# Kernel optimization log

Measured on AMD Instinct MI355X. Metric: run time of the kernel, lower is better.

## Reference

```python
import jax, jax.numpy as jnp
import numpy as np

B, L, DM, DS, DC, E = 2, 1024, 1024, 16, 4, 2
DI = E * DM          # d_inner = 2048
DR = DM // 16        # dt_rank = 64
EPS = 1e-5


def setup_inputs() -> dict:
    key = jax.random.key(0)
    ks = jax.random.split(key, 8)
    s = lambda k, shp, sc: jax.random.normal(k, shp, jnp.float32) * sc
    return {
        "x": s(ks[0], (B, L, DM), 1.0),
        "norm_w": jnp.ones((DM,), jnp.float32),
        "in_proj_w": s(ks[1], (2 * DI, DM), 0.02),
        "conv_w": s(ks[2], (DI, 1, DC), 0.1),        # depthwise kernel [O=DI, I=1, W=DC]
        "conv_b": s(ks[3], (DI,), 0.02),
        "x_proj_w": s(ks[4], (DR + 2 * DS, DI), 0.02),
        "dt_proj_w": s(ks[5], (DI, DR), 0.02),
        "dt_proj_b": s(ks[6], (DI,), 0.02),
        "A_log": jnp.log(jnp.broadcast_to(jnp.arange(1, DS + 1, dtype=jnp.float32), (DI, DS))),
        "D": jnp.ones((DI,), jnp.float32),
        "out_proj_w": s(ks[7], (DM, DI), 0.02),
    }


def reference(x, norm_w, in_proj_w, conv_w, conv_b, x_proj_w,
              dt_proj_w, dt_proj_b, A_log, D, out_proj_w):
    # RMSNorm
    u = x * jax.lax.rsqrt(jnp.mean(x * x, axis=-1, keepdims=True) + EPS) * norm_w

    # in_proj -> [B, L, 2*DI], split into ssm branch and gate
    xz = jnp.einsum('bld,ed->ble', u, in_proj_w)
    xin, z = jnp.split(xz, 2, axis=-1)

    # causal depthwise conv along L + SiLU
    xc = jnp.transpose(xin, (0, 2, 1))                      # [B, DI, L]
    xc = jnp.pad(xc, ((0, 0), (0, 0), (DC - 1, 0)))
    xc = jax.lax.conv_general_dilated(xc, conv_w, (1,), 'VALID',
                                      feature_group_count=DI)  # [B, DI, L]
    xc = jax.nn.silu(xc + conv_b[None, :, None])
    xc = jnp.transpose(xc, (0, 2, 1))                       # [B, L, DI]

    # input-dependent dt, B, C
    dbl = jnp.einsum('bld,ed->ble', xc, x_proj_w)           # [B, L, DR+2*DS]
    dt, Bm, Cm = jnp.split(dbl, [DR, DR + DS], axis=-1)
    delta = jax.nn.softplus(jnp.einsum('blr,dr->bld', dt, dt_proj_w) + dt_proj_b)  # [B,L,DI]

    A = -jnp.exp(A_log)                                     # [DI, DS]
    dA = jnp.exp(delta[..., None] * A)                      # [B, L, DI, DS]
    dBu = delta[..., None] * Bm[:, :, None, :] * xc[..., None]  # [B, L, DI, DS]

    # selective scan: h_t = dA_t * h_{t-1} + dBu_t ; y_t = <h_t, C_t>
    def step(h, inp):
        da, dbu, c = inp
        h = da * h + dbu                                    # [B, DI, DS]
        return h, jnp.einsum('bdn,bn->bd', h, c)

    h0 = jnp.zeros((B, DI, DS), x.dtype)
    _, ys = jax.lax.scan(step, h0,
                         (jnp.swapaxes(dA, 0, 1),
                          jnp.swapaxes(dBu, 0, 1),
                          jnp.swapaxes(Cm, 0, 1)))
    y = jnp.swapaxes(ys, 0, 1) + xc * D                     # [B, L, DI]

    out = jnp.einsum('bld,ed->ble', y * jax.nn.silu(z), out_proj_w)
    return out + x  # residual
```

## Files before the change

kernel.cpp:

```cpp
#include <hip/hip_runtime.h>
#include <math.h>

#define B_   2
#define L_   1024
#define DM   1024
#define DS   16
#define DC   4
#define DI   2048
#define DR   64
#define NTOK (B_*L_)
#define EPSF 1e-5f
#define NC   16
#define CL   (L_/NC)
#define SPLITS 8

typedef __bf16 bf16_t;
typedef bf16_t bf16x4 __attribute__((ext_vector_type(4)));
typedef bf16_t bf16x8 __attribute__((ext_vector_type(8)));
typedef float  f32x4  __attribute__((ext_vector_type(4)));

__device__ __forceinline__ float siluf(float x){ return x / (1.f + __expf(-x)); }
__device__ __forceinline__ float softplusf(float x){ return (x > 20.f) ? x : log1pf(__expf(x)); }

__device__ __forceinline__ void gload_lds16(const void* g, void* l) {
    __builtin_amdgcn_global_load_lds(
        (const __attribute__((address_space(1))) void*)g,
        (__attribute__((address_space(3))) void*)l, 16, 0, 0);
}

__global__ __launch_bounds__(256) void rmsnorm_k(const float* __restrict__ x,
                                                 const float* __restrict__ w,
                                                 bf16_t* __restrict__ uh,
                                                 bf16_t* __restrict__ ul)
{
    int row = blockIdx.x;
    int t = threadIdx.x;
    float4 v = ((const float4*)(x + (size_t)row*DM))[t];
    float ss = v.x*v.x + v.y*v.y + v.z*v.z + v.w*v.w;
    #pragma unroll
    for (int off = 32; off > 0; off >>= 1) ss += __shfl_xor(ss, off, 64);
    __shared__ float sred[4];
    if ((t & 63) == 0) sred[t >> 6] = ss;
    __syncthreads();
    ss = sred[0] + sred[1] + sred[2] + sred[3];
    float rs = rsqrtf(ss * (1.f/(float)DM) + EPSF);
    float4 wv = ((const float4*)w)[t];
    float o[4];
    o[0] = v.x*rs*wv.x; o[1] = v.y*rs*wv.y; o[2] = v.z*rs*wv.z; o[3] = v.w*rs*wv.w;
    bf16x4 hv, lv;
    #pragma unroll
    for (int j = 0; j < 4; ++j) {
        bf16_t h = (bf16_t)o[j];
        hv[j] = h;
        lv[j] = (bf16_t)(o[j] - (float)h);
    }
    *(bf16x4*)(uh + (size_t)row*DM + t*4) = hv;
    *(bf16x4*)(ul + (size_t)row*DM + t*4) = lv;
}

__global__ __launch_bounds__(256) void split_k(const float* __restrict__ s,
                                               bf16_t* __restrict__ h,
                                               bf16_t* __restrict__ l, int n4)
{
    int i = blockIdx.x * 256 + threadIdx.x;
    if (i >= n4) return;
    float4 v = ((const float4*)s)[i];
    float o[4] = {v.x, v.y, v.z, v.w};
    bf16x4 hv, lv;
    #pragma unroll
    for (int j = 0; j < 4; ++j) {
        bf16_t hh = (bf16_t)o[j];
        hv[j] = hh;
        lv[j] = (bf16_t)(o[j] - (float)hh);
    }
    ((bf16x4*)h)[i] = hv;
    ((bf16x4*)l)[i] = lv;
}

__global__ __launch_bounds__(256) void splitx_k(const float* __restrict__ s,
                                                bf16_t* __restrict__ h,
                                                bf16_t* __restrict__ l)
{
    int i = blockIdx.x * 256 + threadIdx.x;
    int row = i >> 9;
    bf16x4 hv, lv;
    if (row < 96) {
        float4 v = ((const float4*)s)[i];
        float o[4] = {v.x, v.y, v.z, v.w};
        #pragma unroll
        for (int j = 0; j < 4; ++j) {
            bf16_t hh = (bf16_t)o[j];
            hv[j] = hh;
            lv[j] = (bf16_t)(o[j] - (float)hh);
        }
    } else {
        #pragma unroll
        for (int j = 0; j < 4; ++j) { hv[j] = (bf16_t)0.f; lv[j] = (bf16_t)0.f; }
    }
    ((bf16x4*)h)[i] = hv;
    ((bf16x4*)l)[i] = lv;
}

template<int BN, int EPI, bool SK>
__global__ __launch_bounds__(256) void gemm_mfma(
    const bf16_t* __restrict__ Ah, const bf16_t* __restrict__ Al,
    const bf16_t* __restrict__ Bh, const bf16_t* __restrict__ Bl,
    float* __restrict__ C, int ldc,
    const float* __restrict__ res, const float* __restrict__ bias,
    int M, int N, int K, int kspl)
{
    constexpr int NJ   = BN / 32;
    constexpr int WN   = BN / 2;
    constexpr int ACH  = 8;
    constexpr int BCH  = BN / 16;
    constexpr int NCH  = 2*ACH + 2*BCH;
    constexpr int PERW = NCH / 4;
    constexpr int AOFF_L = 128*32;
    constexpr int BOFF_H = 2*128*32;
    constexpr int BOFF_L = 2*128*32 + BN*32;
    constexpr int BUFSZ  = 2*128*32 + 2*BN*32;

    __shared__ bf16_t lds[2*BUFSZ];

    int t = threadIdx.x;
    int w = t >> 6, lane = t & 63;
    int wr = w >> 1, wc = w & 1;
    int m0 = blockIdx.y * 128;
    int n0 = SK ? 0 : blockIdx.x * BN;
    int k0beg = SK ? blockIdx.x * kspl : 0;
    int nst = (SK ? kspl : K) >> 5;
    float* Cp = C;
    if (SK) Cp += (size_t)blockIdx.x * M * BN;

    f32x4 acc[4][NJ];
    #pragma unroll
    for (int i = 0; i < 4; ++i)
        #pragma unroll
        for (int j = 0; j < NJ; ++j)
            acc[i][j] = (f32x4){0.f, 0.f, 0.f, 0.f};

    int lrow = lane >> 2;
    int lcol = (lane & 3) * 8;
    int ar   = wr*64 + (lane & 15);
    int br   = wc*WN + (lane & 15);
    int koff = (lane >> 4) * 8;

    auto STAGE = [&](int buf, int k0) {
        int base = buf ? BUFSZ : 0;
        #pragma unroll
        for (int q = 0; q < PERW; ++q) {
            int ch = w * PERW + q;
            const bf16_t* g; int le;
            if (ch < ACH) {
                int cc = ch;
                g  = Ah + (size_t)(m0 + cc*16 + lrow)*K + k0 + lcol;
                le = cc*512 + lane*8;
            } else if (ch < 2*ACH) {
                int cc = ch - ACH;
                g  = Al + (size_t)(m0 + cc*16 + lrow)*K + k0 + lcol;
                le = AOFF_L + cc*512 + lane*8;
            } else if (ch < 2*ACH + BCH) {
                int cc = ch - 2*ACH;
                g  = Bh + (size_t)(n0 + cc*16 + lrow)*K + k0 + lcol;
                le = BOFF_H + cc*512 + lane*8;
            } else {
                int cc = ch - 2*ACH - BCH;
                g  = Bl + (size_t)(n0 + cc*16 + lrow)*K + k0 + lcol;
                le = BOFF_L + cc*512 + lane*8;
            }
            gload_lds16(g, &lds[base + le]);
        }
    };

    STAGE(0, k0beg);
    __syncthreads();
    int cur = 0;
    for (int s = 0; s < nst; ++s) {
        int k0 = k0beg + (s << 5);
        if (s + 1 < nst) STAGE(cur ^ 1, k0 + 32);
        int base = cur ? BUFSZ : 0;

        bf16x8 ah[4], al4[4], bh[NJ], bl4[NJ];
        #pragma unroll
        for (int i = 0; i < 4; ++i) {
            ah[i]  = *(const bf16x8*)&lds[base + (ar + i*16)*32 + koff];
            al4[i] = *(const bf16x8*)&lds[base + AOFF_L + (ar + i*16)*32 + koff];
        }
        #pragma unroll
        for (int j = 0; j < NJ; ++j) {
            bh[j]  = *(const bf16x8*)&lds[base + BOFF_H + (br + j*16)*32 + koff];
            bl4[j] = *(const bf16x8*)&lds[base + BOFF_L + (br + j*16)*32 + koff];
        }
        #pragma unroll
        for (int i = 0; i < 4; ++i)
            #pragma unroll
            for (int j = 0; j < NJ; ++j) {
                acc[i][j] = __builtin_amdgcn_mfma_f32_16x16x32_bf16(ah[i],  bh[j],  acc[i][j], 0, 0, 0);
                acc[i][j] = __builtin_amdgcn_mfma_f32_16x16x32_bf16(al4[i], bh[j],  acc[i][j], 0, 0, 0);
                acc[i][j] = __builtin_amdgcn_mfma_f32_16x16x32_bf16(ah[i],  bl4[j], acc[i][j], 0, 0, 0);
            }
        __syncthreads();
        cur ^= 1;
    }

    int rb = m0 + wr*64 + (lane >> 4)*4;
    int cb = n0 + wc*WN + (lane & 15);
    #pragma unroll
    for (int i = 0; i < 4; ++i)
        #pragma unroll
        for (int j = 0; j < NJ; ++j) {
            int col = cb + j*16;
            float bcol = (EPI == 1) ? bias[col] : 0.f;
            #pragma unroll
            for (int r = 0; r < 4; ++r) {
                int row = rb + i*16 + r;
                float v = acc[i][j][r];
                if (EPI == 1) v = softplusf(v + bcol);
                if (EPI == 2) v += res[(size_t)row*ldc + col];
                Cp[(size_t)row*ldc + col] = v;
            }
        }
}

__global__ __launch_bounds__(256) void xproj_reduce(const float* __restrict__ parts,
                                                    bf16_t* __restrict__ dth,
                                                    bf16_t* __restrict__ dtl,
                                                    float* __restrict__ bc)
{
    int idx = blockIdx.x * 256 + threadIdx.x;
    int m  = idx >> 5;
    int c  = (idx & 31) * 4;
    float4 s = {0.f, 0.f, 0.f, 0.f};
    #pragma unroll
    for (int sp = 0; sp < SPLITS; ++sp) {
        float4 v = *(const float4*)(parts + ((size_t)sp*NTOK + m)*128 + c);
        s.x += v.x; s.y += v.y; s.z += v.z; s.w += v.w;
    }
    if (c < 64) {
        float o[4] = {s.x, s.y, s.z, s.w};
        bf16x4 hv, lv;
        #pragma unroll
        for (int j = 0; j < 4; ++j) {
            bf16_t hh = (bf16_t)o[j];
            hv[j] = hh;
            lv[j] = (bf16_t)(o[j] - (float)hh);
        }
        *(bf16x4*)(dth + (size_t)m*DR + c) = hv;
        *(bf16x4*)(dtl + (size_t)m*DR + c) = lv;
    } else if (c < 96) {
        *(float4*)(bc + (size_t)m*32 + (c - 64)) = s;
    }
}

__global__ __launch_bounds__(256) void conv_silu_k(const float* __restrict__ xz,
                                                   const float* __restrict__ cw,
                                                   const float* __restrict__ cb,
                                                   bf16_t* __restrict__ xch,
                                                   bf16_t* __restrict__ xcl)
{
    int idx = blockIdx.x * 256 + threadIdx.x;
    int d4 = idx & (DI/4 - 1);
    int m  = idx >> 9;
    int l  = m & (L_ - 1);
    int d  = d4 * 4;

    float4 w0 = *(const float4*)(cw + (size_t)(d+0)*DC);
    float4 w1 = *(const float4*)(cw + (size_t)(d+1)*DC);
    float4 w2 = *(const float4*)(cw + (size_t)(d+2)*DC);
    float4 w3 = *(const float4*)(cw + (size_t)(d+3)*DC);
    float wr0[4] = {w0.x,w0.y,w0.z,w0.w};
    float wr1[4] = {w1.x,w1.y,w1.z,w1.w};
    float wr2[4] = {w2.x,w2.y,w2.z,w2.w};
    float wr3[4] = {w3.x,w3.y,w3.z,w3.w};
    float4 bias = *(const float4*)(cb + d);
    float a0 = bias.x, a1 = bias.y, a2 = bias.z, a3 = bias.w;

    #pragma unroll
    for (int j = 0; j < DC; ++j) {
        int tt = l - (DC-1) + j;
        if (tt < 0) continue;
        float4 xv = *(const float4*)(xz + (size_t)(m - l + tt)*(2*DI) + d);
        a0 = fmaf(wr0[j], xv.x, a0);
        a1 = fmaf(wr1[j], xv.y, a1);
        a2 = fmaf(wr2[j], xv.z, a2);
        a3 = fmaf(wr3[j], xv.w, a3);
    }
    float o[4] = { siluf(a0), siluf(a1), siluf(a2), siluf(a3) };
    bf16x4 hv, lv;
    #pragma unroll
    for (int j = 0; j < 4; ++j) {
        bf16_t hh = (bf16_t)o[j];
        hv[j] = hh;
        lv[j] = (bf16_t)(o[j] - (float)hh);
    }
    *(bf16x4*)(xch + (size_t)m*DI + d) = hv;
    *(bf16x4*)(xcl + (size_t)m*DI + d) = lv;
}

__global__ __launch_bounds__(256) void scan_p1(const float* __restrict__ delta,
                                               const bf16_t* __restrict__ xch,
                                               const bf16_t* __restrict__ xcl,
                                               const float* __restrict__ bc,
                                               const float* __restrict__ A_log,
                                               float* __restrict__ Pbuf,
                                               float* __restrict__ Hbuf)
{
    __shared__ float Bsh[CL][16];
    int t = threadIdx.x;
    int blk = blockIdx.x;
    int d = (blk & 7) * 256 + t;
    int c = (blk >> 3) & (NC - 1);
    int b = blk >> 7;
    int m0 = b * L_ + c * CL;

    for (int i = t; i < CL*16; i += 256)
        Bsh[i >> 4][i & 15] = bc[(size_t)(m0 + (i >> 4))*32 + (i & 15)];
    __syncthreads();

    float A[16], h[16];
    #pragma unroll
    for (int j = 0; j < 4; ++j) {
        float4 al = *(const float4*)(A_log + (size_t)d*DS + j*4);
        A[j*4+0] = -__expf(al.x); A[j*4+1] = -__expf(al.y);
        A[j*4+2] = -__expf(al.z); A[j*4+3] = -__expf(al.w);
    }
    #pragma unroll
    for (int n = 0; n < 16; ++n) h[n] = 0.f;
    float S = 0.f;

    #pragma unroll 4
    for (int tt = 0; tt < CL; ++tt) {
        int m = m0 + tt;
        float dv = delta[(size_t)m*DI + d];
        float xv = (float)xch[(size_t)m*DI + d] + (float)xcl[(size_t)m*DI + d];
        float dx = dv * xv;
        S += dv;
        #pragma unroll
        for (int n = 0; n < 16; ++n) {
            float dA = __expf(dv * A[n]);
            h[n] = fmaf(dA, h[n], Bsh[tt][n] * dx);
        }
    }

    size_t o = ((size_t)((b*NC + c)*DI) + d) * DS;
    #pragma unroll
    for (int j = 0; j < 4; ++j) {
        float4 pv, hv;
        pv.x = __expf(A[j*4+0]*S); pv.y = __expf(A[j*4+1]*S);
        pv.z = __expf(A[j*4+2]*S); pv.w = __expf(A[j*4+3]*S);
        hv.x = h[j*4+0]; hv.y = h[j*4+1]; hv.z = h[j*4+2]; hv.w = h[j*4+3];
        *(float4*)(Pbuf + o + j*4) = pv;
        *(float4*)(Hbuf + o + j*4) = hv;
    }
}

__global__ __launch_bounds__(256) void scan_p2(float* Pbuf, const float* __restrict__ Hbuf)
{
    int idx = blockIdx.x * 256 + threadIdx.x;
    int n = idx & 15;
    int d = (idx >> 4) & (DI - 1);
    int b = idx >> 15;
    float h = 0.f;
    #pragma unroll
    for (int c = 0; c < NC; ++c) {
        size_t o = ((size_t)((b*NC + c)*DI) + d) * DS + n;
        float p  = Pbuf[o];
        float hh = Hbuf[o];
        Pbuf[o] = h;
        h = fmaf(p, h, hh);
    }
}

__global__ __launch_bounds__(256) void scan_p3(const float* __restrict__ delta,
                                               const float* __restrict__ xz,
                                               const bf16_t* __restrict__ xch,
                                               const bf16_t* __restrict__ xcl,
                                               const float* __restrict__ bc,
                                               const float* __restrict__ A_log,
                                               const float* __restrict__ Dp,
                                               const float* __restrict__ h0buf,
                                               bf16_t* __restrict__ gh,
                                               bf16_t* __restrict__ gl)
{
    __shared__ float Bsh[CL][16];
    __shared__ float Csh[CL][16];
    int t = threadIdx.x;
    int blk = blockIdx.x;
    int d = (blk & 7) * 256 + t;
    int c = (blk >> 3) & (NC - 1);
    int b = blk >> 7;
    int m0 = b * L_ + c * CL;

    for (int i = t; i < CL*16; i += 256) {
        int tt = i >> 4, n = i & 15;
        size_t ro = (size_t)(m0 + tt)*32;
        Bsh[tt][n] = bc[ro + n];
        Csh[tt][n] = bc[ro + 16 + n];
    }
    __syncthreads();

    float A[16], h[16];
    #pragma unroll
    for (int j = 0; j < 4; ++j) {
        float4 al = *(const float4*)(A_log + (size_t)d*DS + j*4);
        A[j*4+0] = -__expf(al.x); A[j*4+1] = -__expf(al.y);
        A[j*4+2] = -__expf(al.z); A[j*4+3] = -__expf(al.w);
    }
    size_t o = ((size_t)((b*NC + c)*DI) + d) * DS;
    #pragma unroll
    for (int j = 0; j < 4; ++j) {
        float4 hv = *(const float4*)(h0buf + o + j*4);
        h[j*4+0] = hv.x; h[j*4+1] = hv.y; h[j*4+2] = hv.z; h[j*4+3] = hv.w;
    }
    float Dreg = Dp[d];

    for (int t0 = 0; t0 < CL; t0 += 4) {
        float dv[4], xv[4], zv[4];
        #pragma unroll
        for (int q = 0; q < 4; ++q) {
            int m = m0 + t0 + q;
            dv[q] = delta[(size_t)m*DI + d];
            xv[q] = (float)xch[(size_t)m*DI + d] + (float)xcl[(size_t)m*DI + d];
            zv[q] = xz[(size_t)m*(2*DI) + DI + d];
        }
        #pragma unroll
        for (int q = 0; q < 4; ++q) {
            int tt = t0 + q, m = m0 + tt;
            float dx = dv[q] * xv[q];
            float y = 0.f;
            #pragma unroll
            for (int n = 0; n < 16; ++n) {
                float dA = __expf(dv[q] * A[n]);
                h[n] = fmaf(dA, h[n], Bsh[tt][n] * dx);
                y = fmaf(h[n], Csh[tt][n], y);
            }
            float gv = (y + xv[q]*Dreg) * siluf(zv[q]);
            bf16_t hh = (bf16_t)gv;
            gh[(size_t)m*DI + d] = hh;
            gl[(size_t)m*DI + d] = (bf16_t)(gv - (float)hh);
        }
    }
}

extern "C" void kernel_launch(void* const* d_in, const int* in_sizes, int n_in,
                              void* d_out, int out_size, void* d_ws, size_t ws_size,
                              hipStream_t stream)
{
    const float* x         = (const float*)d_in[0];
    const float* norm_w    = (const float*)d_in[1];
    const float* in_proj_w = (const float*)d_in[2];
    const float* conv_w    = (const float*)d_in[3];
    const float* conv_b    = (const float*)d_in[4];
    const float* x_proj_w  = (const float*)d_in[5];
    const float* dt_proj_w = (const float*)d_in[6];
    const float* dt_proj_b = (const float*)d_in[7];
    const float* A_log     = (const float*)d_in[8];
    const float* Dp        = (const float*)d_in[9];
    const float* out_proj_w= (const float*)d_in[10];
    float* out = (float*)d_out;

    char* p = (char*)d_ws;
    float*  xz    = (float*)p;  p += (size_t)NTOK*2*DI*4;
    bf16_t* xch   = (bf16_t*)p; p += (size_t)NTOK*DI*2;
    bf16_t* xcl   = (bf16_t*)p; p += (size_t)NTOK*DI*2;
    float*  delta = (float*)p;  p += (size_t)NTOK*DI*4;
    float*  bc    = (float*)p;  p += (size_t)NTOK*32*4;
    bf16_t* dth   = (bf16_t*)p; p += (size_t)NTOK*DR*2;
    bf16_t* dtl   = (bf16_t*)p; p += (size_t)NTOK*DR*2;
    float*  Hbuf  = (float*)p;  p += (size_t)B_*NC*DI*DS*4;
    float*  Pbuf  = (float*)p;  p += (size_t)B_*NC*DI*DS*4;
    char*   Wreg  = p;          p += (size_t)2*DI*DM*2*2;
    bf16_t* wxh   = (bf16_t*)p; p += (size_t)128*DI*2;
    bf16_t* wxl   = (bf16_t*)p; p += (size_t)128*DI*2;
    bf16_t* wdth  = (bf16_t*)p; p += (size_t)DI*DR*2;
    bf16_t* wdtl  = (bf16_t*)p; p += (size_t)DI*DR*2;

    bf16_t* uh  = (bf16_t*)Pbuf;
    bf16_t* ul  = uh + (size_t)NTOK*DM;
    bf16_t* wih = (bf16_t*)Wreg;
    bf16_t* wil = wih + (size_t)2*DI*DM;
    bf16_t* gh  = (bf16_t*)Wreg;
    bf16_t* gl  = gh + (size_t)NTOK*DI;
    bf16_t* woh = (bf16_t*)delta;
    bf16_t* wol = woh + (size_t)DM*DI;
    float*  parts = Hbuf;

    rmsnorm_k<<<NTOK, 256, 0, stream>>>(x, norm_w, uh, ul);

    split_k<<<(2*DI*DM/4)/256, 256, 0, stream>>>(in_proj_w, wih, wil, 2*DI*DM/4);
    split_k<<<(DI*DR/4)/256, 256, 0, stream>>>(dt_proj_w, wdth, wdtl, DI*DR/4);
    splitx_k<<<(128*DI/4)/256, 256, 0, stream>>>(x_proj_w, wxh, wxl);

    gemm_mfma<128,0,false><<<dim3((2*DI)/128, NTOK/128), 256, 0, stream>>>(
        uh, ul, wih, wil, xz, 2*DI, nullptr, nullptr, NTOK, 2*DI, DM, 0);

    conv_silu_k<<<(NTOK*(DI/4))/256, 256, 0, stream>>>(xz, conv_w, conv_b, xch, xcl);

    gemm_mfma<128,0,true><<<dim3(SPLITS, NTOK/128), 256, 0, stream>>>(
        xch, xcl, wxh, wxl, parts, 128, nullptr, nullptr, NTOK, 128, DI, DI/SPLITS);
    xproj_reduce<<<(NTOK*32)/256, 256, 0, stream>>>(parts, dth, dtl, bc);

    gemm_mfma<128,1,false><<<dim3(DI/128, NTOK/128), 256, 0, stream>>>(
        dth, dtl, wdth, wdtl, delta, DI, nullptr, dt_proj_b, NTOK, DI, DR, 0);

    scan_p1<<<B_*NC*(DI/256), 256, 0, stream>>>(delta, xch, xcl, bc, A_log, Pbuf, Hbuf);
    scan_p2<<<(B_*DI*DS)/256, 256, 0, stream>>>(Pbuf, Hbuf);
    scan_p3<<<B_*NC*(DI/256), 256, 0, stream>>>(delta, xz, xch, xcl, bc, A_log, Dp,
                                                Pbuf, gh, gl);

    split_k<<<(DM*DI/4)/256, 256, 0, stream>>>(out_proj_w, woh, wol, DM*DI/4);

    gemm_mfma<64,2,false><<<dim3(DM/64, NTOK/128), 256, 0, stream>>>(
        gh, gl, woh, wol, out, DM, x, nullptr, NTOK, DM, DI, 0);
}
```

Before: 350.5 us.

## Fuse split kernels, swizzle GEMM LDS access, store chunk delta sums, double scan chunks

Merges the RMSNorm and three weight-split kernels into one launch, and folds the out_proj weight split into the x_proj reduce kernel. The scan now writes only the per-chunk delta sum instead of 16 decay products per channel, recomputing exp in pass 2, and uses 32 chunks instead of 16 for more parallelism. The GEMM's per-lane column offsets get an XOR swizzle meant to reduce LDS bank conflicts. In exchange, pass 2 does extra exp work and serial chunk steps, and the swizzle only stays correct if the staging and read offsets match.

After: 424.6 us. 1.21x slower.

```diff
diff --git a/kernel.cpp b/kernel.cpp
--- a/kernel.cpp
+++ b/kernel.cpp
@@ -10,7 +10,7 @@
 #define DR   64
 #define NTOK (B_*L_)
 #define EPSF 1e-5f
-#define NC   16
+#define NC   32
 #define CL   (L_/NC)
 #define SPLITS 8
 
@@ -28,77 +28,89 @@
         (__attribute__((address_space(3))) void*)l, 16, 0, 0);
 }
 
-__global__ __launch_bounds__(256) void rmsnorm_k(const float* __restrict__ x,
-                                                 const float* __restrict__ w,
-                                                 bf16_t* __restrict__ uh,
-                                                 bf16_t* __restrict__ ul)
-{
-    int row = blockIdx.x;
+struct hl_t { bf16_t h, l; };
+__device__ __forceinline__ hl_t split2(float v) {
+    hl_t r;
+    r.h = (bf16_t)v;
+    r.l = (bf16_t)(v - (float)r.h);
+    return r;
+}
+
+#define SPLIT_IN_BLKS  ((2*DI*DM/4)/256)
+#define SPLIT_DT_BLKS  ((DI*DR/4)/256)
+#define SPLIT_X_BLKS   ((128*DI/4)/256)
+__global__ __launch_bounds__(256) void rms_split_all(
+    const float* __restrict__ x, const float* __restrict__ w,
+    bf16_t* __restrict__ uh, bf16_t* __restrict__ ul,
+    const float* __restrict__ in_w, bf16_t* __restrict__ wih, bf16_t* __restrict__ wil,
+    const float* __restrict__ dt_w, bf16_t* __restrict__ wdth, bf16_t* __restrict__ wdtl,
+    const float* __restrict__ x_w,  bf16_t* __restrict__ wxh,  bf16_t* __restrict__ wxl)
+{
+    __shared__ float sred[4];
+    int blk = blockIdx.x;
     int t = threadIdx.x;
-    float4 v = ((const float4*)(x + (size_t)row*DM))[t];
-    float ss = v.x*v.x + v.y*v.y + v.z*v.z + v.w*v.w;
-    #pragma unroll
-    for (int off = 32; off > 0; off >>= 1) ss += __shfl_xor(ss, off, 64);
-    __shared__ float sred[4];
-    if ((t & 63) == 0) sred[t >> 6] = ss;
-    __syncthreads();
-    ss = sred[0] + sred[1] + sred[2] + sred[3];
-    float rs = rsqrtf(ss * (1.f/(float)DM) + EPSF);
-    float4 wv = ((const float4*)w)[t];
-    float o[4];
-    o[0] = v.x*rs*wv.x; o[1] = v.y*rs*wv.y; o[2] = v.z*rs*wv.z; o[3] = v.w*rs*wv.w;
-    bf16x4 hv, lv;
-    #pragma unroll
-    for (int j = 0; j < 4; ++j) {
-        bf16_t h = (bf16_t)o[j];
-        hv[j] = h;
-        lv[j] = (bf16_t)(o[j] - (float)h);
-    }
-    *(bf16x4*)(uh + (size_t)row*DM + t*4) = hv;
-    *(bf16x4*)(ul + (size_t)row*DM + t*4) = lv;
-}
-
-__global__ __launch_bounds__(256) void split_k(const float* __restrict__ s,
-                                               bf16_t* __restrict__ h,
-                                               bf16_t* __restrict__ l, int n4)
-{
-    int i = blockIdx.x * 256 + threadIdx.x;
-    if (i >= n4) return;
-    float4 v = ((const float4*)s)[i];
-    float o[4] = {v.x, v.y, v.z, v.w};
-    bf16x4 hv, lv;
-    #pragma unroll
-    for (int j = 0; j < 4; ++j) {
-        bf16_t hh = (bf16_t)o[j];
-        hv[j] = hh;
-        lv[j] = (bf16_t)(o[j] - (float)hh);
-    }
-    ((bf16x4*)h)[i] = hv;
-    ((bf16x4*)l)[i] = lv;
-}
-
-__global__ __launch_bounds__(256) void splitx_k(const float* __restrict__ s,
-                                                bf16_t* __restrict__ h,
-                                                bf16_t* __restrict__ l)
-{
-    int i = blockIdx.x * 256 + threadIdx.x;
-    int row = i >> 9;
-    bf16x4 hv, lv;
-    if (row < 96) {
-        float4 v = ((const float4*)s)[i];
+
+    if (blk < NTOK) {
+        int row = blk;
+        float4 v = ((const float4*)(x + (size_t)row*DM))[t];
+        float ss = v.x*v.x + v.y*v.y + v.z*v.z + v.w*v.w;
+        #pragma unroll
+        for (int off = 32; off > 0; off >>= 1) ss += __shfl_xor(ss, off, 64);
+        if ((t & 63) == 0) sred[t >> 6] = ss;
+        __syncthreads();
+        ss = sred[0] + sred[1] + sred[2] + sred[3];
+        float rs = rsqrtf(ss * (1.f/(float)DM) + EPSF);
+        float4 wv = ((const float4*)w)[t];
+        float o[4];
+        o[0] = v.x*rs*wv.x; o[1] = v.y*rs*wv.y; o[2] = v.z*rs*wv.z; o[3] = v.w*rs*wv.w;
+        bf16x4 hv, lv;
+        #pragma unroll
+        for (int j = 0; j < 4; ++j) { hl_t s = split2(o[j]); hv[j] = s.h; lv[j] = s.l; }
+        *(bf16x4*)(uh + (size_t)row*DM + t*4) = hv;
+        *(bf16x4*)(ul + (size_t)row*DM + t*4) = lv;
+        return;
+    }
+    blk -= NTOK;
+    if (blk < SPLIT_IN_BLKS) {
+        int i = blk * 256 + t;
+        float4 v = ((const float4*)in_w)[i];
         float o[4] = {v.x, v.y, v.z, v.w};
-        #pragma unroll
-        for (int j = 0; j < 4; ++j) {
-            bf16_t hh = (bf16_t)o[j];
-            hv[j] = hh;
-            lv[j] = (bf16_t)(o[j] - (float)hh);
-        }
-    } else {
-        #pragma unroll
-        for (int j = 0; j < 4; ++j) { hv[j] = (bf16_t)0.f; lv[j] = (bf16_t)0.f; }
-    }
-    ((bf16x4*)h)[i] = hv;
-    ((bf16x4*)l)[i] = lv;
+        bf16x4 hv, lv;
+        #pragma unroll
+        for (int j = 0; j < 4; ++j) { hl_t s = split2(o[j]); hv[j] = s.h; lv[j] = s.l; }
+        ((bf16x4*)wih)[i] = hv;
+        ((bf16x4*)wil)[i] = lv;
+        return;
+    }
+    blk -= SPLIT_IN_BLKS;
+    if (blk < SPLIT_DT_BLKS) {
+        int i = blk * 256 + t;
+        float4 v = ((const float4*)dt_w)[i];
+        float o[4] = {v.x, v.y, v.z, v.w};
+        bf16x4 hv, lv;
+        #pragma unroll
+        for (int j = 0; j < 4; ++j) { hl_t s = split2(o[j]); hv[j] = s.h; lv[j] = s.l; }
+        ((bf16x4*)wdth)[i] = hv;
+        ((bf16x4*)wdtl)[i] = lv;
+        return;
+    }
+    blk -= SPLIT_DT_BLKS;
+    {
+        int i = blk * 256 + t;
+        int row = i >> 9;
+        bf16x4 hv, lv;
+        if (row < 96) {
+            float4 v = ((const float4*)x_w)[i];
+            float o[4] = {v.x, v.y, v.z, v.w};
+            #pragma unroll
+            for (int j = 0; j < 4; ++j) { hl_t s = split2(o[j]); hv[j] = s.h; lv[j] = s.l; }
+        } else {
+            #pragma unroll
+            for (int j = 0; j < 4; ++j) { hv[j] = (bf16_t)0.f; lv[j] = (bf16_t)0.f; }
+        }
+        ((bf16x4*)wxh)[i] = hv;
+        ((bf16x4*)wxl)[i] = lv;
+    }
 }
 
 template<int BN, int EPI, bool SK>
@@ -140,10 +152,10 @@
             acc[i][j] = (f32x4){0.f, 0.f, 0.f, 0.f};
 
     int lrow = lane >> 2;
-    int lcol = (lane & 3) * 8;
+    int lcol = (((lane & 3) ^ ((lane >> 3) & 3)) * 8);
     int ar   = wr*64 + (lane & 15);
     int br   = wc*WN + (lane & 15);
-    int koff = (lane >> 4) * 8;
+    int koff = (((lane >> 4) ^ ((lane >> 1) & 3)) * 8);
 
     auto STAGE = [&](int buf, int k0) {
         int base = buf ? BUFSZ : 0;
@@ -222,33 +234,47 @@
         }
 }
 
-__global__ __launch_bounds__(256) void xproj_reduce(const float* __restrict__ parts,
-                                                    bf16_t* __restrict__ dth,
-                                                    bf16_t* __restrict__ dtl,
-                                                    float* __restrict__ bc)
-{
-    int idx = blockIdx.x * 256 + threadIdx.x;
-    int m  = idx >> 5;
-    int c  = (idx & 31) * 4;
-    float4 s = {0.f, 0.f, 0.f, 0.f};
-    #pragma unroll
-    for (int sp = 0; sp < SPLITS; ++sp) {
-        float4 v = *(const float4*)(parts + ((size_t)sp*NTOK + m)*128 + c);
-        s.x += v.x; s.y += v.y; s.z += v.z; s.w += v.w;
-    }
-    if (c < 64) {
-        float o[4] = {s.x, s.y, s.z, s.w};
+__global__ __launch_bounds__(256) void reduce_split_o(
+    const float* __restrict__ parts,
+    bf16_t* __restrict__ dth, bf16_t* __restrict__ dtl,
+    float* __restrict__ bc,
+    const float* __restrict__ out_w,
+    bf16_t* __restrict__ woh, bf16_t* __restrict__ wol)
+{
+    int blk = blockIdx.x;
+    int t = threadIdx.x;
+    if (blk < (NTOK*32)/256) {
+        int idx = blk * 256 + t;
+        int m  = idx >> 5;
+        int c  = (idx & 31) * 4;
+        float4 s = {0.f, 0.f, 0.f, 0.f};
+        #pragma unroll
+        for (int sp = 0; sp < SPLITS; ++sp) {
+            float4 v = *(const float4*)(parts + ((size_t)sp*NTOK + m)*128 + c);
+            s.x += v.x; s.y += v.y; s.z += v.z; s.w += v.w;
+        }
+        if (c < 64) {
+            float o[4] = {s.x, s.y, s.z, s.w};
+            bf16x4 hv, lv;
+            #pragma unroll
+            for (int j = 0; j < 4; ++j) { hl_t sp2 = split2(o[j]); hv[j] = sp2.h; lv[j] = sp2.l; }
+            *(bf16x4*)(dth + (size_t)m*DR + c) = hv;
+            *(bf16x4*)(dtl + (size_t)m*DR + c) = lv;
+        } else if (c < 96) {
+            *(float4*)(bc + (size_t)m*32 + (c - 64)) = s;
+        }
+        return;
+    }
+    blk -= (NTOK*32)/256;
+    {
+        int i = blk * 256 + t;
+        float4 v = ((const float4*)out_w)[i];
+        float o[4] = {v.x, v.y, v.z, v.w};
         bf16x4 hv, lv;
         #pragma unroll
-        for (int j = 0; j < 4; ++j) {
-            bf16_t hh = (bf16_t)o[j];
-            hv[j] = hh;
-            lv[j] = (bf16_t)(o[j] - (float)hh);
-        }
-        *(bf16x4*)(dth + (size_t)m*DR + c) = hv;
-        *(bf16x4*)(dtl + (size_t)m*DR + c) = lv;
-    } else if (c < 96) {
-        *(float4*)(bc + (size_t)m*32 + (c - 64)) = s;
+        for (int j = 0; j < 4; ++j) { hl_t s = split2(o[j]); hv[j] = s.h; lv[j] = s.l; }
+        ((bf16x4*)woh)[i] = hv;
+        ((bf16x4*)wol)[i] = lv;
     }
 }
 
@@ -288,11 +314,7 @@
     float o[4] = { siluf(a0), siluf(a1), siluf(a2), siluf(a3) };
     bf16x4 hv, lv;
     #pragma unroll
-    for (int j = 0; j < 4; ++j) {
-        bf16_t hh = (bf16_t)o[j];
-        hv[j] = hh;
-        lv[j] = (bf16_t)(o[j] - (float)hh);
-    }
+    for (int j = 0; j < 4; ++j) { hl_t s = split2(o[j]); hv[j] = s.h; lv[j] = s.l; }
     *(bf16x4*)(xch + (size_t)m*DI + d) = hv;
     *(bf16x4*)(xcl + (size_t)m*DI + d) = lv;
 }
@@ -302,7 +324,7 @@
                                                const bf16_t* __restrict__ xcl,
                                                const float* __restrict__ bc,
                                                const float* __restrict__ A_log,
-                                               float* __restrict__ Pbuf,
+                                               float* __restrict__ Sbuf,
                                                float* __restrict__ Hbuf)
 {
     __shared__ float Bsh[CL][16];
@@ -310,7 +332,7 @@
     int blk = blockIdx.x;
     int d = (blk & 7) * 256 + t;
     int c = (blk >> 3) & (NC - 1);
-    int b = blk >> 7;
+    int b = blk >> 8;
     int m0 = b * L_ + c * CL;
 
     for (int i = t; i < CL*16; i += 256)
@@ -342,32 +364,34 @@
         }
     }
 
+    Sbuf[(size_t)(b*NC + c)*DI + d] = S;
     size_t o = ((size_t)((b*NC + c)*DI) + d) * DS;
     #pragma unroll
     for (int j = 0; j < 4; ++j) {
-        float4 pv, hv;
-        pv.x = __expf(A[j*4+0]*S); pv.y = __expf(A[j*4+1]*S);
-        pv.z = __expf(A[j*4+2]*S); pv.w = __expf(A[j*4+3]*S);
+        float4 hv;
         hv.x = h[j*4+0]; hv.y = h[j*4+1]; hv.z = h[j*4+2]; hv.w = h[j*4+3];
-        *(float4*)(Pbuf + o + j*4) = pv;
         *(float4*)(Hbuf + o + j*4) = hv;
     }
 }
 
-__global__ __launch_bounds__(256) void scan_p2(float* Pbuf, const float* __restrict__ Hbuf)
+__global__ __launch_bounds__(256) void scan_p2(const float* __restrict__ Sbuf,
+                                               float* __restrict__ Hbuf,
+                                               const float* __restrict__ A_log)
 {
     int idx = blockIdx.x * 256 + threadIdx.x;
     int n = idx & 15;
     int d = (idx >> 4) & (DI - 1);
     int b = idx >> 15;
+    float Areg = -__expf(A_log[(size_t)d*DS + n]);
     float h = 0.f;
     #pragma unroll
     for (int c = 0; c < NC; ++c) {
-        size_t o = ((size_t)((b*NC + c)*DI) + d) * DS + n;
-        float p  = Pbuf[o];
+        size_t so = (size_t)(b*NC + c)*DI + d;
+        size_t o  = so * DS + n;
+        float P  = __expf(Areg * Sbuf[so]);
         float hh = Hbuf[o];
-        Pbuf[o] = h;
-        h = fmaf(p, h, hh);
+        Hbuf[o] = h;
+        h = fmaf(P, h, hh);
     }
 }
 
@@ -388,7 +412,7 @@
     int blk = blockIdx.x;
     int d = (blk & 7) * 256 + t;
     int c = (blk >> 3) & (NC - 1);
-    int b = blk >> 7;
+    int b = blk >> 8;
     int m0 = b * L_ + c * CL;
 
     for (int i = t; i < CL*16; i += 256) {
@@ -435,9 +459,9 @@
                 y = fmaf(h[n], Csh[tt][n], y);
             }
             float gv = (y + xv[q]*Dreg) * siluf(zv[q]);
-            bf16_t hh = (bf16_t)gv;
-            gh[(size_t)m*DI + d] = hh;
-            gl[(size_t)m*DI + d] = (bf16_t)(gv - (float)hh);
+            hl_t s = split2(gv);
+            gh[(size_t)m*DI + d] = s.h;
+            gl[(size_t)m*DI + d] = s.l;
         }
     }
 }
@@ -468,28 +492,26 @@
     bf16_t* dth   = (bf16_t*)p; p += (size_t)NTOK*DR*2;
     bf16_t* dtl   = (bf16_t*)p; p += (size_t)NTOK*DR*2;
     float*  Hbuf  = (float*)p;  p += (size_t)B_*NC*DI*DS*4;
-    float*  Pbuf  = (float*)p;  p += (size_t)B_*NC*DI*DS*4;
     char*   Wreg  = p;          p += (size_t)2*DI*DM*2*2;
+    bf16_t* woh   = (bf16_t*)p; p += (size_t)DM*DI*2;
+    bf16_t* wol   = (bf16_t*)p; p += (size_t)DM*DI*2;
+    float*  Sbuf  = (float*)p;  p += (size_t)B_*NC*DI*4;
     bf16_t* wxh   = (bf16_t*)p; p += (size_t)128*DI*2;
     bf16_t* wxl   = (bf16_t*)p; p += (size_t)128*DI*2;
     bf16_t* wdth  = (bf16_t*)p; p += (size_t)DI*DR*2;
     bf16_t* wdtl  = (bf16_t*)p; p += (size_t)DI*DR*2;
 
-    bf16_t* uh  = (bf16_t*)Pbuf;
+    bf16_t* uh  = (bf16_t*)Hbuf;
     bf16_t* ul  = uh + (size_t)NTOK*DM;
+    float*  parts = Hbuf;
     bf16_t* wih = (bf16_t*)Wreg;
     bf16_t* wil = wih + (size_t)2*DI*DM;
     bf16_t* gh  = (bf16_t*)Wreg;
     bf16_t* gl  = gh + (size_t)NTOK*DI;
-    bf16_t* woh = (bf16_t*)delta;
-    bf16_t* wol = woh + (size_t)DM*DI;
-    float*  parts = Hbuf;
-
-    rmsnorm_k<<<NTOK, 256, 0, stream>>>(x, norm_w, uh, ul);
-
-    split_k<<<(2*DI*DM/4)/256, 256, 0, stream>>>(in_proj_w, wih, wil, 2*DI*DM/4);
-    split_k<<<(DI*DR/4)/256, 256, 0, stream>>>(dt_proj_w, wdth, wdtl, DI*DR/4);
-    splitx_k<<<(128*DI/4)/256, 256, 0, stream>>>(x_proj_w, wxh, wxl);
+
+    rms_split_all<<<NTOK + SPLIT_IN_BLKS + SPLIT_DT_BLKS + SPLIT_X_BLKS, 256, 0, stream>>>(
+        x, norm_w, uh, ul, in_proj_w, wih, wil,
+        dt_proj_w, wdth, wdtl, x_proj_w, wxh, wxl);
 
     gemm_mfma<128,0,false><<<dim3((2*DI)/128, NTOK/128), 256, 0, stream>>>(
         uh, ul, wih, wil, xz, 2*DI, nullptr, nullptr, NTOK, 2*DI, DM, 0);
@@ -498,17 +520,17 @@
 
     gemm_mfma<128,0,true><<<dim3(SPLITS, NTOK/128), 256, 0, stream>>>(
         xch, xcl, wxh, wxl, parts, 128, nullptr, nullptr, NTOK, 128, DI, DI/SPLITS);
-    xproj_reduce<<<(NTOK*32)/256, 256, 0, stream>>>(parts, dth, dtl, bc);
+
+    reduce_split_o<<<(NTOK*32)/256 + (DM*DI/4)/256, 256, 0, stream>>>(
+        parts, dth, dtl, bc, out_proj_w, woh, wol);
 
     gemm_mfma<128,1,false><<<dim3(DI/128, NTOK/128), 256, 0, stream>>>(
         dth, dtl, wdth, wdtl, delta, DI, nullptr, dt_proj_b, NTOK, DI, DR, 0);
 
-    scan_p1<<<B_*NC*(DI/256), 256, 0, stream>>>(delta, xch, xcl, bc, A_log, Pbuf, Hbuf);
-    scan_p2<<<(B_*DI*DS)/256, 256, 0, stream>>>(Pbuf, Hbuf);
+    scan_p1<<<B_*NC*(DI/256), 256, 0, stream>>>(delta, xch, xcl, bc, A_log, Sbuf, Hbuf);
+    scan_p2<<<(B_*DI*DS)/256, 256, 0, stream>>>(Sbuf, Hbuf, A_log);
     scan_p3<<<B_*NC*(DI/256), 256, 0, stream>>>(delta, xz, xch, xcl, bc, A_log, Dp,
-                                                Pbuf, gh, gl);
-
-    split_k<<<(DM*DI/4)/256, 256, 0, stream>>>(out_proj_w, woh, wol, DM*DI/4);
+                                                Hbuf, gh, gl);
 
     gemm_mfma<64,2,false><<<dim3(DM/64, NTOK/128), 256, 0, stream>>>(
         gh, gl, woh, wol, out, DM, x, nullptr, NTOK, DM, DI, 0);
```
